# Kernel tuning notes

Measured on AMD Instinct MI355X. Metric: run time of the kernel, lower is better.

Reference implementation:

```python
import jax, jax.numpy as jnp
import numpy as np

BETA = 100.0
# (in_ch, out_ch) for the 12 effective 1x1-conv layers. ResNeXt blocks are
# fused: all branches read the same block input, so stacking branch weights
# along out-channels gives one GEMM per block.
LAYER_DIMS = [(259, 515), (515, 512), (512, 512), (512, 576), (576, 576),
              (576, 768), (768, 768), (768, 768), (768, 960), (960, 960),
              (960, 896), (896, 1)]


def setup_inputs() -> dict:
    key = jax.random.key(0)
    keys = jax.random.split(key, 2 + len(LAYER_DIMS))
    B, N = 2, 8192
    inp = {
        "input": jax.random.normal(keys[0], (B, N, 3), dtype=jnp.float32),
        "latent": jax.random.normal(keys[1], (B, 256), dtype=jnp.float32),
    }
    for i, (cin, cout) in enumerate(LAYER_DIMS):
        std = np.sqrt(2.0) / np.sqrt(cin)
        inp[f"W{i+1}"] = std * jax.random.normal(keys[2 + i], (cout, cin), dtype=jnp.float32)
        inp[f"b{i+1}"] = jnp.zeros((cout,), dtype=jnp.float32)
    return inp


def _sp(z):
    # torch Softplus(beta=100): softplus(beta*z)/beta (jax.nn.softplus is stable)
    return jax.nn.softplus(BETA * z) / BETA


def reference(input, latent,
              W1, b1, W2, b2, W3, b3, W4, b4, W5, b5, W6, b6,
              W7, b7, W8, b8, W9, b9, W10, b10, W11, b11, W12, b12):
    B, N, _ = input.shape
    lat = jnp.broadcast_to(latent[:, None, :], (B, N, latent.shape[-1]))
    x = jnp.concatenate([input, lat], axis=-1)  # (B, N, 259)
    input_con = x

    # layer 1: conv + softplus, grad seeded from first 3 input columns (xyz)
    z = x @ W1.T + b1                                   # (B, N, 515)
    g = jax.nn.sigmoid(BETA * z)[..., None] * W1[:, :3]  # (B, N, 515, 3)
    x = _sp(z)

    mids = [(W2, b2), (W3, b3), (W4, b4), (W5, b5), (W6, b6), (W7, b7),
            (W8, b8), (W9, b9), (W10, b10), (W11, b11)]
    for W, b in mids:  # fixed small layer loop (10 fused ResNeXt blocks)
        z = x @ W.T + b                                 # (B, N, Cout)
        g = jax.nn.sigmoid(BETA * z)[..., None] * jnp.einsum('oc,bnci->bnoi', W, g)
        x = _sp(z)

    # final 1x1 conv, no activation
    z = x @ W12.T + b12                                 # (B, N, 1)
    g = jnp.einsum('oc,bnci->bnoi', W12, g)             # (B, N, 1, 3)
    # torch returns conv output channel-first: (B, 1, N)
    return (z.transpose(0, 2, 1), g, input_con)
```

## Files before the change

### kernel.cpp

```cpp
#include <hip/hip_runtime.h>
#include <math.h>


typedef unsigned short u16;
typedef _Float16 f16;
typedef f16   f16x8  __attribute__((ext_vector_type(8)));
typedef float f32x16 __attribute__((ext_vector_type(16)));

__device__ __forceinline__ u16   f2h(float x){ return __builtin_bit_cast(u16, (f16)x); }
__device__ __forceinline__ float h2f(u16 b){ return (float)__builtin_bit_cast(f16, b); }

__device__ __forceinline__ void glld16(const void* g, void* l){
  __builtin_amdgcn_global_load_lds(
      (const __attribute__((address_space(1))) unsigned*)g,
      (__attribute__((address_space(3))) unsigned*)l, 16, 0, 0);
}

template<int N> __device__ __forceinline__ void wait_vmcnt(){
  static_assert(N == 0 || N == 3 || N == 6, "unsupported vmcnt literal");
  if constexpr (N == 0) asm volatile("s_waitcnt vmcnt(0)" ::: "memory");
  if constexpr (N == 3) asm volatile("s_waitcnt vmcnt(3)" ::: "memory");
  if constexpr (N == 6) asm volatile("s_waitcnt vmcnt(6)" ::: "memory");
}

__device__ __forceinline__ void xcd_map(int& bx, int& by){
  const int gx = gridDim.x, gy = gridDim.y;
  const int nwg = gx * gy;
  const int d   = by * gx + bx;
  if ((nwg & 7) == 0){
    const int q = nwg >> 3;
    const int t = (d & 7) * q + (d >> 3);
    by = t % gy;
    bx = t / gy;
  }
}

template<bool LAST>
__global__ __launch_bounds__(256, 3)
void fwd_layer(const u16* __restrict__ Sin, long long psIn, int kpad,
               u16* __restrict__ SoutX, long long psOut,
               u16* __restrict__ Gout, int opitch,
               const u16* __restrict__ Wh, const u16* __restrict__ Wl,
               const float* __restrict__ bias, const float* __restrict__ w12,
               int cout)
{
  __shared__ u16 As[2][2][4][64][8];
  __shared__ u16 Bs[2][2][4][128][8];

  int bx = blockIdx.x, by = blockIdx.y;
  xcd_map(bx, by);

  const int tid   = threadIdx.x;
  const int w     = tid >> 6;
  const int lane  = tid & 63;
  const int lrow  = lane & 31;
  const int lhalf = lane >> 5;
  const int mh    = w >> 1;
  const int oh    = w & 1;
  const int m0    = bx * 64;
  const int o0    = by * 128;

  f32x16 zinit = {};
  f32x16 accx[2];
  accx[0] = zinit; accx[1] = zinit;

  const u16* aSrc[2];
  #pragma unroll
  for (int p = 0; p < 2; ++p)
    aSrc[p] = Sin + (long long)p * psIn + (long long)(m0 + lane) * kpad + w * 8;
  const u16* bSrc[2][2];
  #pragma unroll
  for (int h = 0; h < 2; ++h){
    const u16* Wx = h ? Wl : Wh;
    #pragma unroll
    for (int hf = 0; hf < 2; ++hf)
      bSrc[h][hf] = Wx + (long long)(o0 + hf*64 + lane) * kpad + w * 8;
  }

  auto stage = [&](int buf, int kElem){
    #pragma unroll
    for (int p = 0; p < 2; ++p)
      glld16(aSrc[p] + kElem, &As[buf][p][w][0][0]);
    #pragma unroll
    for (int h = 0; h < 2; ++h)
      #pragma unroll
      for (int hf = 0; hf < 2; ++hf)
        glld16(bSrc[h][hf] + kElem, &Bs[buf][h][w][hf*64][0]);
  };

  auto compute = [&](int buf){
    __builtin_amdgcn_s_setprio(1);
    #pragma unroll
    for (int s = 0; s < 2; ++s){
      const int kq = s*2 + lhalf;
      f16x8 a0 = *(const f16x8*)&As[buf][0][kq][mh*32 + lrow][0];
      f16x8 a1 = *(const f16x8*)&As[buf][1][kq][mh*32 + lrow][0];
      #pragma unroll
      for (int f = 0; f < 2; ++f){
        const int oc = oh*64 + f*32 + lrow;
        f16x8 bh = *(const f16x8*)&Bs[buf][0][kq][oc][0];
        f16x8 bl = *(const f16x8*)&Bs[buf][1][kq][oc][0];
        accx[f] = __builtin_amdgcn_mfma_f32_32x32x16_f16(a0, bh, accx[f], 0,0,0);
        accx[f] = __builtin_amdgcn_mfma_f32_32x32x16_f16(a1, bh, accx[f], 0,0,0);
        accx[f] = __builtin_amdgcn_mfma_f32_32x32x16_f16(a0, bl, accx[f], 0,0,0);
      }
    }
    __builtin_amdgcn_s_setprio(0);
  };

  const int nk = kpad >> 5;
  stage(0, 0);
  stage(1, 32);
  int cur = 0;
  for (int t = 0; t < nk - 1; ++t){
    wait_vmcnt<6>();
    __builtin_amdgcn_s_barrier();
    compute(cur);
    asm volatile("s_waitcnt lgkmcnt(0)" ::: "memory");
    __builtin_amdgcn_s_barrier();
    if (t + 2 < nk) stage(cur, (t + 2) * 32);
    cur ^= 1;
  }
  wait_vmcnt<0>();
  __builtin_amdgcn_s_barrier();
  compute(cur);

  const int mb = m0 + mh*32;
  #pragma unroll
  for (int f = 0; f < 2; ++f){
    const int o = o0 + oh*64 + f*32 + lrow;
    if (o >= opitch) continue;
    const bool real = (o < cout);
    const float bo  = real ? bias[o] : 0.f;
    const float wf  = (LAST && real) ? w12[o] : 0.f;
    #pragma unroll
    for (int r = 0; r < 16; ++r){
      const int m = mb + (r & 3) + ((r >> 2) << 3) + (lhalf << 2);
      const float z    = accx[f][r] + bo;
      const float gate = 1.f / (1.f + expf(-100.f * z));
      const float sp   = fmaxf(z, 0.f) + 0.01f * log1pf(expf(-100.f * fabsf(z)));
      const long long idx = (long long)m * opitch + o;
      const u16 xh = f2h(sp);
      SoutX[idx]         = xh;
      SoutX[psOut + idx] = f2h(sp - h2f(xh));
      float gv;
      if (LAST) gv = gate * wf;
      else      gv = real ? gate : 0.f;
      Gout[idx] = f2h(gv);
    }
  }
}

__global__ __launch_bounds__(256, 4)
void bwd_layer(const u16* __restrict__ Vin, int kpad,
               u16* __restrict__ Vout, int opitch,
               const u16* __restrict__ Gprev, const u16* __restrict__ Wt)
{
  __shared__ u16 As[2][4][64][8];
  __shared__ u16 Bs[2][4][128][8];

  int bx = blockIdx.x, by = blockIdx.y;
  xcd_map(bx, by);

  const int tid   = threadIdx.x;
  const int w     = tid >> 6;
  const int lane  = tid & 63;
  const int lrow  = lane & 31;
  const int lhalf = lane >> 5;
  const int mh    = w >> 1;
  const int oh    = w & 1;
  const int m0    = bx * 64;
  const int o0    = by * 128;

  f32x16 zinit = {};
  f32x16 acc[2];
  acc[0] = zinit; acc[1] = zinit;

  const u16* aSrc = Vin + (long long)(m0 + lane) * kpad + w * 8;
  const u16* bSrc[2];
  #pragma unroll
  for (int hf = 0; hf < 2; ++hf)
    bSrc[hf] = Wt + (long long)(o0 + hf*64 + lane) * kpad + w * 8;

  auto stage = [&](int buf, int kElem){
    glld16(aSrc + kElem, &As[buf][w][0][0]);
    #pragma unroll
    for (int hf = 0; hf < 2; ++hf)
      glld16(bSrc[hf] + kElem, &Bs[buf][w][hf*64][0]);
  };

  auto compute = [&](int buf){
    __builtin_amdgcn_s_setprio(1);
    #pragma unroll
    for (int s = 0; s < 2; ++s){
      const int kq = s*2 + lhalf;
      f16x8 a = *(const f16x8*)&As[buf][kq][mh*32 + lrow][0];
      #pragma unroll
      for (int f = 0; f < 2; ++f){
        const int oc = oh*64 + f*32 + lrow;
        f16x8 b = *(const f16x8*)&Bs[buf][kq][oc][0];
        acc[f] = __builtin_amdgcn_mfma_f32_32x32x16_f16(a, b, acc[f], 0,0,0);
      }
    }
    __builtin_amdgcn_s_setprio(0);
  };

  const int nk = kpad >> 5;
  stage(0, 0);
  stage(1, 32);
  int cur = 0;
  for (int t = 0; t < nk - 1; ++t){
    wait_vmcnt<3>();
    __builtin_amdgcn_s_barrier();
    compute(cur);
    asm volatile("s_waitcnt lgkmcnt(0)" ::: "memory");
    __builtin_amdgcn_s_barrier();
    if (t + 2 < nk) stage(cur, (t + 2) * 32);
    cur ^= 1;
  }
  wait_vmcnt<0>();
  __builtin_amdgcn_s_barrier();
  compute(cur);

  const int mb = m0 + mh*32;
  #pragma unroll
  for (int f = 0; f < 2; ++f){
    const int o = o0 + oh*64 + f*32 + lrow;
    if (o >= opitch) continue;
    #pragma unroll
    for (int r = 0; r < 16; ++r){
      const int m = mb + (r & 3) + ((r >> 2) << 3) + (lhalf << 2);
      const long long idx = (long long)m * opitch + o;
      Vout[idx] = f2h(acc[f][r] * h2f(Gprev[idx]));
    }
  }
}

__global__ __launch_bounds__(256)
void final_z(const u16* __restrict__ Sx, long long ps, int kpad,
             const float* __restrict__ W12, const float* __restrict__ b12,
             float* __restrict__ out1, int cin, int mBase)
{
  const int lane = threadIdx.x & 63;
  const int wv   = threadIdx.x >> 6;
  const int m = blockIdx.x * 4 + wv;
  const u16* row = Sx + (long long)m * kpad;
  float s = 0.f;
  for (int c = lane; c < cin; c += 64)
    s += (h2f(row[c]) + h2f(row[ps + c])) * W12[c];
  #pragma unroll
  for (int off = 32; off > 0; off >>= 1) s += __shfl_xor(s, off);
  if (lane == 0) out1[mBase + m] = s + b12[0];
}

__global__ __launch_bounds__(256)
void final_g(const u16* __restrict__ V0, int kpad,
             const float* __restrict__ W1, int cinW,
             float* __restrict__ out2, int width, int mBase)
{
  const int lane = threadIdx.x & 63;
  const int wv   = threadIdx.x >> 6;
  const int m = blockIdx.x * 4 + wv;
  const u16* row = V0 + (long long)m * kpad;
  float g0 = 0.f, g1 = 0.f, g2 = 0.f;
  for (int o = lane; o < width; o += 64){
    const float v = h2f(row[o]);
    const float* wr = W1 + (long long)o * cinW;
    g0 += v * wr[0]; g1 += v * wr[1]; g2 += v * wr[2];
  }
  #pragma unroll
  for (int off = 32; off > 0; off >>= 1){
    g0 += __shfl_xor(g0, off); g1 += __shfl_xor(g1, off); g2 += __shfl_xor(g2, off);
  }
  if (lane == 0){
    float* g = out2 + (long long)(mBase + m) * 3;
    g[0] = g0; g[1] = g1; g[2] = g2;
  }
}

__global__ void prep_input(const float* __restrict__ input,
                           const float* __restrict__ latent,
                           float* __restrict__ out3,
                           u16* __restrict__ x0, long long psX0, int N)
{
  const int m = blockIdx.x;
  const int b = m / N;
  const int c = threadIdx.x;
  if (c >= 288) return;
  float v = 0.f;
  if (c < 3) v = input[(long long)m*3 + c];
  else if (c < 259) v = latent[(long long)b*256 + (c - 3)];
  if (c < 259) out3[(long long)m*259 + c] = v;
  const u16 h = f2h(v);
  x0[(long long)m*288 + c]        = h;
  x0[psX0 + (long long)m*288 + c] = f2h(v - h2f(h));
}

__global__ void split_w(const float* __restrict__ W, u16* __restrict__ wh,
                        u16* __restrict__ wl, int cout, int cin, int kpad, int total)
{
  const int idx = blockIdx.x * 256 + threadIdx.x;
  if (idx >= total) return;
  const int o = idx / kpad, c = idx % kpad;
  const float v = (o < cout && c < cin) ? W[(long long)o*cin + c] : 0.f;
  const u16 h = f2h(v);
  wh[idx] = h;
  wl[idx] = f2h(v - h2f(h));
}

__global__ void split_wt(const float* __restrict__ W, u16* __restrict__ wt,
                         int cout, int cin, int kpad, int total)
{
  const int idx = blockIdx.x * 256 + threadIdx.x;
  if (idx >= total) return;
  const int c = idx / kpad, k = idx % kpad;
  const float v = (c < cin && k < cout) ? W[(long long)k*cin + c] : 0.f;
  wt[idx] = f2h(v);
}

extern "C" void kernel_launch(void* const* d_in, const int* in_sizes, int n_in,
                              void* d_out, int out_size, void* d_ws, size_t ws_size,
                              hipStream_t stream)
{
  static const int CIN [12] = {259,515,512,512,576,576,768,768,768,960,960,896};
  static const int COUT[12] = {515,512,512,576,576,768,768,768,960,960,896,1};
  int PF[11], KPF[11], NYF[11], NYB[11];
  for (int j = 0; j < 11; ++j){
    PF[j]  = (COUT[j] + 31) & ~31;
    KPF[j] = (j == 0) ? 288 : PF[j-1];
    NYF[j] = (COUT[j] + 127) / 128;
    NYB[j] = (CIN[j] + 127) / 128;
  }

  const float* input  = (const float*)d_in[0];
  const float* latent = (const float*)d_in[1];
  auto Wp = [&](int j){ return (const float*)d_in[2 + 2*j]; };
  auto Bp = [&](int j){ return (const float*)d_in[3 + 2*j]; };

  const int Bn = in_sizes[1] / 256;
  const int Nn = in_sizes[0] / (3 * Bn);
  const int M  = Bn * Nn;

  float* out1 = (float*)d_out;
  float* out2 = out1 + M;
  float* out3 = out2 + (size_t)M * 3;

  char* wsp = (char*)d_ws;
  u16 *WH[11], *WL[11], *WT[11];
  for (int j = 0; j < 11; ++j){
    const size_t sz = (size_t)NYF[j] * 128 * KPF[j] * 2;
    WH[j] = (u16*)wsp; wsp += sz;
    WL[j] = (u16*)wsp; wsp += sz;
  }
  for (int j = 1; j < 11; ++j){
    const size_t sz = (size_t)NYB[j] * 128 * PF[j] * 2;
    WT[j] = (u16*)wsp; wsp += sz;
  }
  u16* x0 = (u16*)wsp;
  const long long psX0 = (long long)M * 288;
  wsp += (size_t)2 * psX0 * 2;

  size_t sumPF = 0;
  for (int j = 0; j < 11; ++j) sumPF += (size_t)PF[j];
  const size_t used   = (size_t)(wsp - (char*)d_ws);
  const size_t remain = (ws_size > used) ? (ws_size - used) : 0;
  const size_t perPoint = sumPF * 2 + (size_t)2 * 2 * 960 * 2;
  long long pc = (long long)(remain / perPoint);
  pc &= ~63LL;
  int Pc = (int)((pc < (long long)M) ? pc : (long long)M);
  if (Pc < 64) Pc = 64;

  u16* gates[11];
  for (int j = 0; j < 11; ++j){
    gates[j] = (u16*)wsp; wsp += (size_t)Pc * PF[j] * 2;
  }
  u16* bufA = (u16*)wsp;
  u16* bufB = bufA + (size_t)2 * Pc * 960;
  u16* vA = bufB;
  u16* vB = bufB + (size_t)Pc * 960;

  prep_input<<<M, 320, 0, stream>>>(input, latent, out3, x0, psX0, Nn);
  for (int j = 0; j < 11; ++j){
    const int total = NYF[j] * 128 * KPF[j];
    split_w<<<(total + 255)/256, 256, 0, stream>>>(
        Wp(j), WH[j], WL[j], COUT[j], CIN[j], KPF[j], total);
  }
  for (int j = 1; j < 11; ++j){
    const int total = NYB[j] * 128 * PF[j];
    split_wt<<<(total + 255)/256, 256, 0, stream>>>(
        Wp(j), WT[j], COUT[j], CIN[j], PF[j], total);
  }

  for (int cm0 = 0; cm0 < M; cm0 += Pc){
    const int Mc = (M - cm0 < Pc) ? (M - cm0) : Pc;
    const int gx = Mc / 64;

    u16* src = x0 + (long long)cm0 * 288;
    long long psSrc = psX0;
    int kp = 288;
    u16* dstTbl[2] = { bufA, bufB };
    for (int j = 0; j < 11; ++j){
      u16* dst = dstTbl[j & 1];
      dim3 g(gx, NYF[j]);
      if (j == 10)
        fwd_layer<true><<<g, 256, 0, stream>>>(
            src, psSrc, kp, dst, (long long)Pc * PF[j], gates[j], PF[j],
            WH[j], WL[j], Bp(j), Wp(11), COUT[j]);
      else
        fwd_layer<false><<<g, 256, 0, stream>>>(
            src, psSrc, kp, dst, (long long)Pc * PF[j], gates[j], PF[j],
            WH[j], WL[j], Bp(j), nullptr, COUT[j]);
      src = dst; psSrc = (long long)Pc * PF[j]; kp = PF[j];
    }

    final_z<<<Mc/4, 256, 0, stream>>>(
        src, psSrc, kp, Wp(11), Bp(11), out1, CIN[11], cm0);

    u16* vin = gates[10];
    for (int j = 10; j >= 1; --j){
      u16* vout = (j & 1) ? vB : vA;
      dim3 g(gx, NYB[j]);
      bwd_layer<<<g, 256, 0, stream>>>(
          vin, PF[j], vout, PF[j-1], gates[j-1], WT[j]);
      vin = vout;
    }

    final_g<<<Mc/4, 256, 0, stream>>>(
        vin, PF[0], Wp(0), CIN[0], out2, COUT[0], cm0);
  }
}
```

Baseline: 2.705 ms.

## Retile forward and backward GEMMs to 8-wave 128-row blocks

The forward kernel now uses 512-thread blocks covering 128 points by 64 output channels, with each wave owning one 32x32 tile. The backward kernel uses 128x128 tiles with 8 waves. The async LDS staging is redistributed so each wave issues 3 (forward) or 2 (backward) global-to-LDS loads per k-step, and the vmcnt waits are adjusted to match. The intent is more waves per CU for latency hiding and better reuse of the A tile across output columns. In exchange, each forward wave holds less accumulator work, and the point chunk size must now be a multiple of 128.

```diff
diff --git a/kernel.cpp b/kernel.cpp
--- a/kernel.cpp
+++ b/kernel.cpp
@@ -17,10 +17,10 @@
 }
 
 template<int N> __device__ __forceinline__ void wait_vmcnt(){
-  static_assert(N == 0 || N == 3 || N == 6, "unsupported vmcnt literal");
+  static_assert(N == 0 || N == 2 || N == 3, "unsupported vmcnt literal");
   if constexpr (N == 0) asm volatile("s_waitcnt vmcnt(0)" ::: "memory");
+  if constexpr (N == 2) asm volatile("s_waitcnt vmcnt(2)" ::: "memory");
   if constexpr (N == 3) asm volatile("s_waitcnt vmcnt(3)" ::: "memory");
-  if constexpr (N == 6) asm volatile("s_waitcnt vmcnt(6)" ::: "memory");
 }
 
 __device__ __forceinline__ void xcd_map(int& bx, int& by){
@@ -36,7 +36,7 @@
 }
 
 template<bool LAST>
-__global__ __launch_bounds__(256, 3)
+__global__ __launch_bounds__(512, 6)
 void fwd_layer(const u16* __restrict__ Sin, long long psIn, int kpad,
                u16* __restrict__ SoutX, long long psOut,
                u16* __restrict__ Gout, int opitch,
@@ -44,48 +44,47 @@
                const float* __restrict__ bias, const float* __restrict__ w12,
                int cout)
 {
-  __shared__ u16 As[2][2][4][64][8];
-  __shared__ u16 Bs[2][2][4][128][8];
+  __shared__ u16 As[2][2][4][128][8];
+  __shared__ u16 Bs[2][2][4][64][8];
 
   int bx = blockIdx.x, by = blockIdx.y;
   xcd_map(bx, by);
 
   const int tid   = threadIdx.x;
-  const int w     = tid >> 6;
+  const int w     = __builtin_amdgcn_readfirstlane(tid >> 6);
   const int lane  = tid & 63;
   const int lrow  = lane & 31;
   const int lhalf = lane >> 5;
   const int mh    = w >> 1;
-  const int oh    = w & 1;
-  const int m0    = bx * 64;
-  const int o0    = by * 128;
-
-  f32x16 zinit = {};
-  f32x16 accx[2];
-  accx[0] = zinit; accx[1] = zinit;
-
-  const u16* aSrc[2];
-  #pragma unroll
-  for (int p = 0; p < 2; ++p)
-    aSrc[p] = Sin + (long long)p * psIn + (long long)(m0 + lane) * kpad + w * 8;
-  const u16* bSrc[2][2];
-  #pragma unroll
-  for (int h = 0; h < 2; ++h){
-    const u16* Wx = h ? Wl : Wh;
-    #pragma unroll
-    for (int hf = 0; hf < 2; ++hf)
-      bSrc[h][hf] = Wx + (long long)(o0 + hf*64 + lane) * kpad + w * 8;
+  const int on    = w & 1;
+  const int m0    = bx * 128;
+  const int o0    = by * 64;
+
+  f32x16 accx = {};
+
+  const u16* gp[3];
+  u16* lp[3];
+  int  bstr[3];
+  #pragma unroll
+  for (int j = 0; j < 3; ++j){
+    const int c = 3 * w + j;
+    if (c < 16){
+      const int pl = c >> 3, rem = c & 7, kq = rem >> 1, rs = rem & 1;
+      gp[j]   = Sin + (long long)pl * psIn + (long long)(m0 + rs*64 + lane) * kpad + kq * 8;
+      lp[j]   = &As[0][pl][kq][rs*64][0];
+      bstr[j] = 2*4*128*8;
+    } else {
+      const int b = c - 16, h = b >> 2, kq = b & 3;
+      gp[j]   = (h ? Wl : Wh) + (long long)(o0 + lane) * kpad + kq * 8;
+      lp[j]   = &Bs[0][h][kq][0][0];
+      bstr[j] = 2*4*64*8;
+    }
   }
 
   auto stage = [&](int buf, int kElem){
     #pragma unroll
-    for (int p = 0; p < 2; ++p)
-      glld16(aSrc[p] + kElem, &As[buf][p][w][0][0]);
-    #pragma unroll
-    for (int h = 0; h < 2; ++h)
-      #pragma unroll
-      for (int hf = 0; hf < 2; ++hf)
-        glld16(bSrc[h][hf] + kElem, &Bs[buf][h][w][hf*64][0]);
+    for (int j = 0; j < 3; ++j)
+      glld16(gp[j] + kElem, lp[j] + buf * bstr[j]);
   };
 
   auto compute = [&](int buf){
@@ -95,112 +94,11 @@
       const int kq = s*2 + lhalf;
       f16x8 a0 = *(const f16x8*)&As[buf][0][kq][mh*32 + lrow][0];
       f16x8 a1 = *(const f16x8*)&As[buf][1][kq][mh*32 + lrow][0];
-      #pragma unroll
-      for (int f = 0; f < 2; ++f){
-        const int oc = oh*64 + f*32 + lrow;
-        f16x8 bh = *(const f16x8*)&Bs[buf][0][kq][oc][0];
-        f16x8 bl = *(const f16x8*)&Bs[buf][1][kq][oc][0];
-        accx[f] = __builtin_amdgcn_mfma_f32_32x32x16_f16(a0, bh, accx[f], 0,0,0);
-        accx[f] = __builtin_amdgcn_mfma_f32_32x32x16_f16(a1, bh, accx[f], 0,0,0);
-        accx[f] = __builtin_amdgcn_mfma_f32_32x32x16_f16(a0, bl, accx[f], 0,0,0);
-      }
-    }
-    __builtin_amdgcn_s_setprio(0);
-  };
-
-  const int nk = kpad >> 5;
-  stage(0, 0);
-  stage(1, 32);
-  int cur = 0;
-  for (int t = 0; t < nk - 1; ++t){
-    wait_vmcnt<6>();
-    __builtin_amdgcn_s_barrier();
-    compute(cur);
-    asm volatile("s_waitcnt lgkmcnt(0)" ::: "memory");
-    __builtin_amdgcn_s_barrier();
-    if (t + 2 < nk) stage(cur, (t + 2) * 32);
-    cur ^= 1;
-  }
-  wait_vmcnt<0>();
-  __builtin_amdgcn_s_barrier();
-  compute(cur);
-
-  const int mb = m0 + mh*32;
-  #pragma unroll
-  for (int f = 0; f < 2; ++f){
-    const int o = o0 + oh*64 + f*32 + lrow;
-    if (o >= opitch) continue;
-    const bool real = (o < cout);
-    const float bo  = real ? bias[o] : 0.f;
-    const float wf  = (LAST && real) ? w12[o] : 0.f;
-    #pragma unroll
-    for (int r = 0; r < 16; ++r){
-      const int m = mb + (r & 3) + ((r >> 2) << 3) + (lhalf << 2);
-      const float z    = accx[f][r] + bo;
-      const float gate = 1.f / (1.f + expf(-100.f * z));
-      const float sp   = fmaxf(z, 0.f) + 0.01f * log1pf(expf(-100.f * fabsf(z)));
-      const long long idx = (long long)m * opitch + o;
-      const u16 xh = f2h(sp);
-      SoutX[idx]         = xh;
-      SoutX[psOut + idx] = f2h(sp - h2f(xh));
-      float gv;
-      if (LAST) gv = gate * wf;
-      else      gv = real ? gate : 0.f;
-      Gout[idx] = f2h(gv);
-    }
-  }
-}
-
-__global__ __launch_bounds__(256, 4)
-void bwd_layer(const u16* __restrict__ Vin, int kpad,
-               u16* __restrict__ Vout, int opitch,
-               const u16* __restrict__ Gprev, const u16* __restrict__ Wt)
-{
-  __shared__ u16 As[2][4][64][8];
-  __shared__ u16 Bs[2][4][128][8];
-
-  int bx = blockIdx.x, by = blockIdx.y;
-  xcd_map(bx, by);
-
-  const int tid   = threadIdx.x;
-  const int w     = tid >> 6;
-  const int lane  = tid & 63;
-  const int lrow  = lane & 31;
-  const int lhalf = lane >> 5;
-  const int mh    = w >> 1;
-  const int oh    = w & 1;
-  const int m0    = bx * 64;
-  const int o0    = by * 128;
-
-  f32x16 zinit = {};
-  f32x16 acc[2];
-  acc[0] = zinit; acc[1] = zinit;
-
-  const u16* aSrc = Vin + (long long)(m0 + lane) * kpad + w * 8;
-  const u16* bSrc[2];
-  #pragma unroll
-  for (int hf = 0; hf < 2; ++hf)
-    bSrc[hf] = Wt + (long long)(o0 + hf*64 + lane) * kpad + w * 8;
-
-  auto stage = [&](int buf, int kElem){
-    glld16(aSrc + kElem, &As[buf][w][0][0]);
-    #pragma unroll
-    for (int hf = 0; hf < 2; ++hf)
-      glld16(bSrc[hf] + kElem, &Bs[buf][w][hf*64][0]);
-  };
-
-  auto compute = [&](int buf){
-    __builtin_amdgcn_s_setprio(1);
-    #pragma unroll
-    for (int s = 0; s < 2; ++s){
-      const int kq = s*2 + lhalf;
-      f16x8 a = *(const f16x8*)&As[buf][kq][mh*32 + lrow][0];
-      #pragma unroll
-      for (int f = 0; f < 2; ++f){
-        const int oc = oh*64 + f*32 + lrow;
-        f16x8 b = *(const f16x8*)&Bs[buf][kq][oc][0];
-        acc[f] = __builtin_amdgcn_mfma_f32_32x32x16_f16(a, b, acc[f], 0,0,0);
-      }
+      f16x8 bh = *(const f16x8*)&Bs[buf][0][kq][on*32 + lrow][0];
+      f16x8 bl = *(const f16x8*)&Bs[buf][1][kq][on*32 + lrow][0];
+      accx = __builtin_amdgcn_mfma_f32_32x32x16_f16(a0, bh, accx, 0,0,0);
+      accx = __builtin_amdgcn_mfma_f32_32x32x16_f16(a1, bh, accx, 0,0,0);
+      accx = __builtin_amdgcn_mfma_f32_32x32x16_f16(a0, bl, accx, 0,0,0);
     }
     __builtin_amdgcn_s_setprio(0);
   };
@@ -222,10 +120,112 @@
   __builtin_amdgcn_s_barrier();
   compute(cur);
 
+  const int o = o0 + on*32 + lrow;
+  if (o >= opitch) return;
+  const bool real = (o < cout);
+  const float bo  = real ? bias[o] : 0.f;
+  const float wf  = (LAST && real) ? w12[o] : 0.f;
   const int mb = m0 + mh*32;
   #pragma unroll
+  for (int r = 0; r < 16; ++r){
+    const int m = mb + (r & 3) + ((r >> 2) << 3) + (lhalf << 2);
+    const float z    = accx[r] + bo;
+    const float gate = 1.f / (1.f + expf(-100.f * z));
+    const float sp   = fmaxf(z, 0.f) + 0.01f * log1pf(expf(-100.f * fabsf(z)));
+    const long long idx = (long long)m * opitch + o;
+    const u16 xh = f2h(sp);
+    SoutX[idx]         = xh;
+    SoutX[psOut + idx] = f2h(sp - h2f(xh));
+    float gv;
+    if (LAST) gv = gate * wf;
+    else      gv = real ? gate : 0.f;
+    Gout[idx] = f2h(gv);
+  }
+}
+
+__global__ __launch_bounds__(512, 8)
+void bwd_layer(const u16* __restrict__ Vin, int kpad,
+               u16* __restrict__ Vout, int opitch,
+               const u16* __restrict__ Gprev, const u16* __restrict__ Wt)
+{
+  __shared__ u16 As[2][4][128][8];
+  __shared__ u16 Bs[2][4][128][8];
+
+  int bx = blockIdx.x, by = blockIdx.y;
+  xcd_map(bx, by);
+
+  const int tid   = threadIdx.x;
+  const int w     = __builtin_amdgcn_readfirstlane(tid >> 6);
+  const int lane  = tid & 63;
+  const int lrow  = lane & 31;
+  const int lhalf = lane >> 5;
+  const int mh    = w >> 1;
+  const int on    = w & 1;
+  const int m0    = bx * 128;
+  const int o0    = by * 128;
+
+  f32x16 acc[2];
+  acc[0] = f32x16{}; acc[1] = f32x16{};
+
+  const u16* gp[2];
+  u16* lp[2];
+  #pragma unroll
+  for (int j = 0; j < 2; ++j){
+    const int c = 2 * w + j;
+    if (c < 8){
+      const int kq = c >> 1, rs = c & 1;
+      gp[j] = Vin + (long long)(m0 + rs*64 + lane) * kpad + kq * 8;
+      lp[j] = &As[0][kq][rs*64][0];
+    } else {
+      const int b = c - 8, kq = b >> 1, rs = b & 1;
+      gp[j] = Wt + (long long)(o0 + rs*64 + lane) * kpad + kq * 8;
+      lp[j] = &Bs[0][kq][rs*64][0];
+    }
+  }
+  const int bstr = 4*128*8;
+
+  auto stage = [&](int buf, int kElem){
+    #pragma unroll
+    for (int j = 0; j < 2; ++j)
+      glld16(gp[j] + kElem, lp[j] + buf * bstr);
+  };
+
+  auto compute = [&](int buf){
+    __builtin_amdgcn_s_setprio(1);
+    #pragma unroll
+    for (int s = 0; s < 2; ++s){
+      const int kq = s*2 + lhalf;
+      f16x8 a = *(const f16x8*)&As[buf][kq][mh*32 + lrow][0];
+      #pragma unroll
+      for (int f = 0; f < 2; ++f){
+        f16x8 b = *(const f16x8*)&Bs[buf][kq][on*64 + f*32 + lrow][0];
+        acc[f] = __builtin_amdgcn_mfma_f32_32x32x16_f16(a, b, acc[f], 0,0,0);
+      }
+    }
+    __builtin_amdgcn_s_setprio(0);
+  };
+
+  const int nk = kpad >> 5;
+  stage(0, 0);
+  stage(1, 32);
+  int cur = 0;
+  for (int t = 0; t < nk - 1; ++t){
+    wait_vmcnt<2>();
+    __builtin_amdgcn_s_barrier();
+    compute(cur);
+    asm volatile("s_waitcnt lgkmcnt(0)" ::: "memory");
+    __builtin_amdgcn_s_barrier();
+    if (t + 2 < nk) stage(cur, (t + 2) * 32);
+    cur ^= 1;
+  }
+  wait_vmcnt<0>();
+  __builtin_amdgcn_s_barrier();
+  compute(cur);
+
+  const int mb = m0 + mh*32;
+  #pragma unroll
   for (int f = 0; f < 2; ++f){
-    const int o = o0 + oh*64 + f*32 + lrow;
+    const int o = o0 + on*64 + f*32 + lrow;
     if (o >= opitch) continue;
     #pragma unroll
     for (int r = 0; r < 16; ++r){
@@ -328,7 +328,7 @@
   for (int j = 0; j < 11; ++j){
     PF[j]  = (COUT[j] + 31) & ~31;
     KPF[j] = (j == 0) ? 288 : PF[j-1];
-    NYF[j] = (COUT[j] + 127) / 128;
+    NYF[j] = (COUT[j] + 63) / 64;
     NYB[j] = (CIN[j] + 127) / 128;
   }
 
@@ -348,7 +348,7 @@
   char* wsp = (char*)d_ws;
   u16 *WH[11], *WL[11], *WT[11];
   for (int j = 0; j < 11; ++j){
-    const size_t sz = (size_t)NYF[j] * 128 * KPF[j] * 2;
+    const size_t sz = (size_t)NYF[j] * 64 * KPF[j] * 2;
     WH[j] = (u16*)wsp; wsp += sz;
     WL[j] = (u16*)wsp; wsp += sz;
   }
@@ -366,9 +366,9 @@
   const size_t remain = (ws_size > used) ? (ws_size - used) : 0;
   const size_t perPoint = sumPF * 2 + (size_t)2 * 2 * 960 * 2;
   long long pc = (long long)(remain / perPoint);
-  pc &= ~63LL;
+  pc &= ~127LL;
   int Pc = (int)((pc < (long long)M) ? pc : (long long)M);
-  if (Pc < 64) Pc = 64;
+  if (Pc < 128) Pc = 128;
 
   u16* gates[11];
   for (int j = 0; j < 11; ++j){
@@ -381,7 +381,7 @@
 
   prep_input<<<M, 320, 0, stream>>>(input, latent, out3, x0, psX0, Nn);
   for (int j = 0; j < 11; ++j){
-    const int total = NYF[j] * 128 * KPF[j];
+    const int total = NYF[j] * 64 * KPF[j];
     split_w<<<(total + 255)/256, 256, 0, stream>>>(
         Wp(j), WH[j], WL[j], COUT[j], CIN[j], KPF[j], total);
   }
@@ -393,7 +393,7 @@
 
   for (int cm0 = 0; cm0 < M; cm0 += Pc){
     const int Mc = (M - cm0 < Pc) ? (M - cm0) : Pc;
-    const int gx = Mc / 64;
+    const int gx = Mc / 128;
 
     u16* src = x0 + (long long)cm0 * 288;
     long long psSrc = psX0;
@@ -403,11 +403,11 @@
       u16* dst = dstTbl[j & 1];
       dim3 g(gx, NYF[j]);
       if (j == 10)
-        fwd_layer<true><<<g, 256, 0, stream>>>(
+        fwd_layer<true><<<g, 512, 0, stream>>>(
             src, psSrc, kp, dst, (long long)Pc * PF[j], gates[j], PF[j],
             WH[j], WL[j], Bp(j), Wp(11), COUT[j]);
       else
-        fwd_layer<false><<<g, 256, 0, stream>>>(
+        fwd_layer<false><<<g, 512, 0, stream>>>(
             src, psSrc, kp, dst, (long long)Pc * PF[j], gates[j], PF[j],
             WH[j], WL[j], Bp(j), nullptr, COUT[j]);
       src = dst; psSrc = (long long)Pc * PF[j]; kp = PF[j];
@@ -420,7 +420,7 @@
     for (int j = 10; j >= 1; --j){
       u16* vout = (j & 1) ? vB : vA;
       dim3 g(gx, NYB[j]);
-      bwd_layer<<<g, 256, 0, stream>>>(
+      bwd_layer<<<g, 512, 0, stream>>>(
           vin, PF[j], vout, PF[j-1], gates[j-1], WT[j]);
       vin = vout;
     }
```

Result: faster. 2.531 ms (-6.4%).
